# Optimization experiments

Hardware: AMD Instinct MI355X
Metric: run time of the kernel (lower is better)

Reference implementation:

```python
import jax, jax.numpy as jnp
import numpy as np

KSIZE = 5      # equivalent steerable kernel size
KMAX = 3       # max circular harmonic
STRIDE = 2
N_IN, N_OUT = 32, 16
B_TOTAL = 3 + 2 * KMAX  # 3 radial atoms at k=0, 2 per harmonic k>=1


def _make_basis():
    # Radial steerable base: Gaussian rings x circular harmonics cos(k*theta)/sin(k*theta)
    ys, xs = np.mgrid[:KSIZE, :KSIZE].astype(np.float64) - (KSIZE - 1) / 2
    r = np.sqrt(xs ** 2 + ys ** 2)
    th = np.arctan2(ys, xs)
    ring = lambda r0: np.exp(-(r - r0) ** 2 / (2 * 0.6 ** 2))
    b0 = np.stack([ring(r0) for r0 in (0.0, 1.0, 2.0)])          # (3, 5, 5)
    br, bi = [], []
    for k in range(1, KMAX + 1):
        br.append(np.stack([ring(r0) * np.cos(k * th) for r0 in (1.0, 2.0)]))  # (2,5,5)
        bi.append(np.stack([ring(r0) * np.sin(k * th) for r0 in (1.0, 2.0)]))
    return (b0.astype(np.float32),
            [b.astype(np.float32) for b in br],
            [b.astype(np.float32) for b in bi])


def _conv_transpose(x, w):
    # torch conv_transpose2d (stride=2, padding='same' -> pad=2, output_padding=1)
    # == dilated-input conv with spatially flipped kernel, explicit pad (2,3).
    rhs = jnp.flip(w, axis=(2, 3))  # (o, i, kh, kw)
    return jax.lax.conv_general_dilated(
        x, rhs, window_strides=(1, 1), padding=((2, 3), (2, 3)),
        lhs_dilation=(STRIDE, STRIDE),
        dimension_numbers=('NCHW', 'OIHW', 'NCHW'))


def setup_inputs() -> dict:
    key = jax.random.key(0)
    k1, k2, k3, k4 = jax.random.split(key, 4)
    x = jax.random.normal(k1, (8, N_IN, 192, 192), jnp.float32)
    # alpha[0]=cos-like, alpha[1]=sin-like field at output resolution; not unit-norm,
    # rho is derived from its norm (rho=None path of forward()).
    alpha = jax.random.normal(k2, (2, 8, 1, 384, 384), jnp.float32)
    weights = jax.random.normal(k3, (N_OUT, N_IN, B_TOTAL), jnp.float32) / np.sqrt(N_IN * B_TOTAL)
    bias = jax.random.normal(k4, (N_OUT,), jnp.float32) * 0.05
    return {"x": x, "alpha": alpha, "weights": weights, "bias": bias}


def reference(x, alpha, weights, bias):
    b0, br, bi = _make_basis()
    # normalize_vector: rho = |alpha|, alpha <- alpha / rho
    rho = jnp.sqrt(jnp.sum(alpha * alpha, axis=0))          # (b, 1, Ho, Wo)
    au = alpha / (rho[None] + 1e-8)
    c1, s1 = au[0], au[1]                                    # cos(a), sin(a)
    # k=0 term (rotation invariant)
    out = _conv_transpose(x, jnp.einsum('oib,bhw->oihw', weights[:, :, :3], jnp.asarray(b0)))
    ck, sk = c1, s1
    off = 3
    for k in range(KMAX):  # harmonics k=1..KMAX, steered by cos(k a), sin(k a)
        wk = weights[:, :, off:off + 2]
        off += 2
        Kr = jnp.einsum('oib,bhw->oihw', wk, jnp.asarray(br[k]))
        Ki = jnp.einsum('oib,bhw->oihw', wk, jnp.asarray(bi[k]))
        out = out + _conv_transpose(x, Kr) * ck + _conv_transpose(x, Ki) * sk
        ckn = ck * c1 - sk * s1  # Chebyshev-style recurrence for cos/sin of (k+1)a
        skn = sk * c1 + ck * s1
        ck, sk = ckn, skn
    return rho * out + bias[None, :, None, None]
```

## Files before the change

### kernel.cpp

```cpp
#include <hip/hip_runtime.h>

#define HIN 192
#define WOUT 384
#define NIN 32
#define NOUT 16
#define NSLOT 9
#define HP 194
#define HPLANE (HP * HP)
#define HQBATCH ((size_t)HPLANE * 18)

typedef float v2f __attribute__((ext_vector_type(2)));

__device__ __forceinline__ unsigned short f2bf(float f) {
    union { float f; unsigned int u; } v; v.f = f;
    unsigned int r = v.u + 0x7fffu + ((v.u >> 16) & 1u);
    return (unsigned short)(r >> 16);
}
__device__ __forceinline__ v2f up2(unsigned u) {
    v2f r;
    r.x = __uint_as_float(u << 16);
    r.y = __uint_as_float(u);
    return r;
}

__global__ __launch_bounds__(256) void kprep_w(const float* __restrict__ w, float* __restrict__ Wt) {
    int t = blockIdx.x * 256 + threadIdx.x;
    if (t >= NIN * NSLOT * NOUT) return;
    int c = t >> 8, r = t & 255;
    int i = r >> 3, j = r & 7;
    int m = c * 8 + j;
    int s = m >> 4, o = m & 15;
    Wt[t] = w[(o * NIN + i) * NSLOT + s];
}

__global__ __launch_bounds__(256) void kzero(uint4* __restrict__ hq, int nb) {
    int t = blockIdx.x * 256 + threadIdx.x;
    if (t >= nb * 772) return;
    int b = t / 772, r = t % 772;
    int iy, ix;
    if (r < 194)      { iy = 0;           ix = r; }
    else if (r < 388) { iy = 193;         ix = r - 194; }
    else if (r < 580) { iy = r - 388 + 1; ix = 0; }
    else              { iy = r - 580 + 1; ix = 193; }
    uint4* p = hq + (size_t)b * HQBATCH + iy * HP + ix;
    uint4 z; z.x = 0; z.y = 0; z.z = 0; z.w = 0;
    #pragma unroll
    for (int c = 0; c < 18; ++c) p[(size_t)c * HPLANE] = z;
}

__global__ __launch_bounds__(256) void kA(const float* __restrict__ x,
                                          const float* __restrict__ Wt,
                                          uint4* __restrict__ hq, int n0) {
    const int b = blockIdx.y;
    const int n = n0 + b;
    const int px = blockIdx.x * 256 + threadIdx.x;
    const int iy = px / HIN, ix = px % HIN;
    const float* xp = x + (size_t)n * NIN * HIN * HIN + px;
    float xv[NIN];
    #pragma unroll
    for (int i = 0; i < NIN; ++i) xv[i] = xp[(size_t)i * HIN * HIN];
    const int pos = (iy + 1) * HP + (ix + 1);
    uint4* hb = hq + (size_t)b * HQBATCH;
    #pragma unroll 1
    for (int c = 0; c < 18; ++c) {
        const float* wc = Wt + c * 256;
        float a[8];
        #pragma unroll
        for (int j = 0; j < 8; ++j) a[j] = 0.0f;
        #pragma unroll
        for (int i = 0; i < NIN; ++i) {
            const float xi = xv[i];
            #pragma unroll
            for (int j = 0; j < 8; ++j) a[j] = fmaf(wc[i * 8 + j], xi, a[j]);
        }
        uint4 v;
        v.x = (unsigned)f2bf(a[0]) | ((unsigned)f2bf(a[1]) << 16);
        v.y = (unsigned)f2bf(a[2]) | ((unsigned)f2bf(a[3]) << 16);
        v.z = (unsigned)f2bf(a[4]) | ((unsigned)f2bf(a[5]) << 16);
        v.w = (unsigned)f2bf(a[6]) | ((unsigned)f2bf(a[7]) << 16);
        hb[(size_t)c * HPLANE + pos] = v;
    }
}

template<int PY, int PX, int HF>
__device__ __forceinline__ void kb_body(const uint4* __restrict__ hb,
                                        const float* __restrict__ alpha,
                                        const float* __restrict__ bias_,
                                        float (&stage)[2][16][128],
                                        const float2 (&Cb)[NSLOT][25],
                                        int n, int Y, int X, int lane) {
    const int oy = 2 * Y + PY, ox = 2 * X + PX;
    const int aoff = (n * WOUT + oy) * WOUT + ox;
    const float a0 = alpha[aoff];
    const float a1 = alpha[(size_t)8 * WOUT * WOUT + aoff];
    const float rr = sqrtf(a0 * a0 + a1 * a1);
    const float inv = 1.0f / (rr + 1e-8f);
    float cc[3], ss[3];
    cc[0] = a0 * inv;                      ss[0] = a1 * inv;
    cc[1] = cc[0] * cc[0] - ss[0] * ss[0]; ss[1] = 2.0f * cc[0] * ss[0];
    cc[2] = cc[1] * cc[0] - ss[1] * ss[0]; ss[2] = ss[1] * cc[0] + cc[1] * ss[0];

    v2f acc2[4];
    #pragma unroll
    for (int j = 0; j < 4; ++j) { acc2[j].x = 0.0f; acc2[j].y = 0.0f; }

    #pragma unroll 1
    for (int ty = 0; ty < 3 - PY; ++ty) {
        const int piy = Y + 2 - ty;
        #pragma unroll 1
        for (int tx = 0; tx < 3 - PX; ++tx) {
            const int pix = X + 2 - tx;
            const int bi = (PY + 2 * ty) * 5 + (PX + 2 * tx);
            const unsigned pos = (unsigned)(piy * HP + pix);
            #pragma unroll
            for (int s = 0; s < NSLOT; ++s) {
                const float2 C = Cb[s][bi];
                float eb;
                if      (s < 3) eb = C.x;
                else if (s < 5) eb = C.x * cc[0] + C.y * ss[0];
                else if (s < 7) eb = C.x * cc[1] + C.y * ss[1];
                else            eb = C.x * cc[2] + C.y * ss[2];
                const uint4 v = hb[(size_t)(2 * s + HF) * HPLANE + pos];
                v2f e2; e2.x = eb; e2.y = eb;
                acc2[0] += e2 * up2(v.x);
                acc2[1] += e2 * up2(v.y);
                acc2[2] += e2 * up2(v.z);
                acc2[3] += e2 * up2(v.w);
            }
        }
    }

    #pragma unroll
    for (int j = 0; j < 4; ++j) {
        stage[PY][HF * 8 + 2 * j + 0][2 * lane + PX] = rr * acc2[j].x + bias_[HF * 8 + 2 * j + 0];
        stage[PY][HF * 8 + 2 * j + 1][2 * lane + PX] = rr * acc2[j].y + bias_[HF * 8 + 2 * j + 1];
    }
}

__global__ __launch_bounds__(512, 4) void kB(const uint4* __restrict__ hq,
                                             const float* __restrict__ alpha,
                                             const float* __restrict__ bias,
                                             float* __restrict__ out, int n0, int nb) {
    __shared__ float2 Cb[NSLOT][25];
    __shared__ float stage[2][16][128];
    {
        const int q = threadIdx.x;
        if (q < NSLOT * 25) {
            int s = q / 25, p = q % 25;
            int ky = p / 5, kx = p % 5;
            float ys = (float)(ky - 2), xs = (float)(kx - 2);
            float r = sqrtf(xs * xs + ys * ys);
            float th = atan2f(ys, xs);
            float cr, ci;
            if (s < 3) {
                float d = r - (float)s;
                cr = expf(-d * d * (1.0f / 0.72f));
                ci = 0.0f;
            } else {
                int k = (s - 3) / 2 + 1;
                float r0 = ((s - 3) & 1) ? 2.0f : 1.0f;
                float d = r - r0;
                float ring = expf(-d * d * (1.0f / 0.72f));
                float a = (float)k * th;
                cr = ring * cosf(a);
                ci = ring * sinf(a);
            }
            Cb[s][p] = make_float2(cr, ci);
        }
    }
    __syncthreads();

    const int tot = gridDim.x;
    const int cpx = tot >> 3;
    const int swz = ((int)blockIdx.x & 7) * cpx + ((int)blockIdx.x >> 3);
    const int Y = swz % 192;
    const int rest = swz / 192;
    const int b = rest % nb;
    const int bx = rest / nb;

    const int n = n0 + b;
    const int lane = threadIdx.x & 63;
    const int wv = threadIdx.x >> 6;
    const int X0 = bx * 64;
    const int X = X0 + lane;
    const uint4* hb = hq + (size_t)b * HQBATCH;

    switch (wv) {
        case 0: kb_body<0, 0, 0>(hb, alpha, bias, stage, Cb, n, Y, X, lane); break;
        case 1: kb_body<0, 1, 0>(hb, alpha, bias, stage, Cb, n, Y, X, lane); break;
        case 2: kb_body<1, 0, 0>(hb, alpha, bias, stage, Cb, n, Y, X, lane); break;
        case 3: kb_body<1, 1, 0>(hb, alpha, bias, stage, Cb, n, Y, X, lane); break;
        case 4: kb_body<0, 0, 1>(hb, alpha, bias, stage, Cb, n, Y, X, lane); break;
        case 5: kb_body<0, 1, 1>(hb, alpha, bias, stage, Cb, n, Y, X, lane); break;
        case 6: kb_body<1, 0, 1>(hb, alpha, bias, stage, Cb, n, Y, X, lane); break;
        default: kb_body<1, 1, 1>(hb, alpha, bias, stage, Cb, n, Y, X, lane); break;
    }

    __syncthreads();

    #pragma unroll
    for (int q = 0; q < 8; ++q) {
        const int f = q * 512 + threadIdx.x;
        const int row = f >> 7, col = f & 127;
        const int py = row >> 4, o = row & 15;
        out[(((size_t)n * NOUT + o) * WOUT + (2 * Y + py)) * WOUT + 2 * X0 + col]
            = stage[py][o][col];
    }
}

__global__ __launch_bounds__(256) void steered_convT(
    const float* __restrict__ x, const float* __restrict__ alpha,
    const float* __restrict__ weights, const float* __restrict__ bias,
    float* __restrict__ out) {
    __shared__ float sb[15 * 25];
    for (int q = threadIdx.x; q < 375; q += 256) {
        int s = q / 25, p = q % 25;
        int ky = p / 5, kx = p % 5;
        float ys = (float)(ky - 2), xs = (float)(kx - 2);
        float r = sqrtf(xs * xs + ys * ys);
        float th = atan2f(ys, xs);
        float val;
        if (s < 3) { float d = r - (float)s; val = expf(-d * d * (1.0f / 0.72f)); }
        else {
            int k = (s - 3) / 4 + 1; int rem = (s - 3) & 3;
            float r0 = (rem & 1) ? 2.0f : 1.0f; float d = r - r0;
            float ring = expf(-d * d * (1.0f / 0.72f));
            float ang = (float)k * th;
            val = ring * ((rem < 2) ? cosf(ang) : sinf(ang));
        }
        sb[q] = val;
    }
    __syncthreads();
    int idx = blockIdx.x * 256 + threadIdx.x;
    int ox = idx % WOUT; int tt = idx / WOUT; int oy = tt % WOUT; int n = tt / WOUT;
    const int plane = WOUT * WOUT;
    int aoff = (n * WOUT + oy) * WOUT + ox;
    float a0 = alpha[aoff], a1 = alpha[8 * plane + aoff];
    float rho = sqrtf(a0 * a0 + a1 * a1);
    float inv = 1.0f / (rho + 1e-8f);
    float c1 = a0 * inv, s1 = a1 * inv;
    float c2 = c1 * c1 - s1 * s1, s2 = 2.0f * s1 * c1;
    float c3 = c2 * c1 - s2 * s1, s3 = s2 * c1 + c2 * s1;
    int py = oy & 1, px = ox & 1;
    int iy0 = (oy >> 1) + 1, ix0 = (ox >> 1) + 1;
    float eb[9][9]; int off[9];
    #pragma unroll
    for (int t = 0; t < 9; ++t) {
        int ty = t / 3, tx = t % 3;
        int ky = py + 2 * ty, kx = px + 2 * tx;
        int iy = iy0 - ty, ix = ix0 - tx;
        bool v = (ky < 5) && (kx < 5) && (iy >= 0) && (iy < HIN) && (ix >= 0) && (ix < HIN);
        float m = v ? 1.0f : 0.0f;
        int ciy = min(max(iy, 0), HIN - 1), cix = min(max(ix, 0), HIN - 1);
        off[t] = ciy * HIN + cix;
        int bi_ = min(ky, 4) * 5 + min(kx, 4);
        eb[0][t] = sb[0 * 25 + bi_] * m;
        eb[1][t] = sb[1 * 25 + bi_] * m;
        eb[2][t] = sb[2 * 25 + bi_] * m;
        eb[3][t] = (sb[3 * 25 + bi_] * c1 + sb[5 * 25 + bi_] * s1) * m;
        eb[4][t] = (sb[4 * 25 + bi_] * c1 + sb[6 * 25 + bi_] * s1) * m;
        eb[5][t] = (sb[7 * 25 + bi_] * c2 + sb[9 * 25 + bi_] * s2) * m;
        eb[6][t] = (sb[8 * 25 + bi_] * c2 + sb[10 * 25 + bi_] * s2) * m;
        eb[7][t] = (sb[11 * 25 + bi_] * c3 + sb[13 * 25 + bi_] * s3) * m;
        eb[8][t] = (sb[12 * 25 + bi_] * c3 + sb[14 * 25 + bi_] * s3) * m;
    }
    float acc[NOUT];
    #pragma unroll
    for (int o = 0; o < NOUT; ++o) acc[o] = 0.0f;
    const float* xn = x + (size_t)n * NIN * HIN * HIN;
    for (int i = 0; i < NIN; ++i) {
        const float* xp = xn + (size_t)i * HIN * HIN;
        float tap[9];
        #pragma unroll
        for (int t = 0; t < 9; ++t) tap[t] = xp[off[t]];
        float G[9];
        #pragma unroll
        for (int b = 0; b < 9; ++b) {
            float s = 0.0f;
            #pragma unroll
            for (int t = 0; t < 9; ++t) s += eb[b][t] * tap[t];
            G[b] = s;
        }
        const float* wp = weights + i * 9;
        #pragma unroll
        for (int o = 0; o < NOUT; ++o) {
            float s = acc[o];
            #pragma unroll
            for (int b = 0; b < 9; ++b) s += wp[o * NIN * 9 + b] * G[b];
            acc[o] = s;
        }
    }
    #pragma unroll
    for (int o = 0; o < NOUT; ++o)
        out[((size_t)(n * NOUT + o) * WOUT + oy) * WOUT + ox] = rho * acc[o] + bias[o];
}

extern "C" void kernel_launch(void* const* d_in, const int* in_sizes, int n_in,
                              void* d_out, int out_size, void* d_ws, size_t ws_size,
                              hipStream_t stream) {
    const float* x       = (const float*)d_in[0];
    const float* alpha   = (const float*)d_in[1];
    const float* weights = (const float*)d_in[2];
    const float* bias    = (const float*)d_in[3];
    float* out = (float*)d_out;

    const size_t hoff = 32768;
    const size_t perb = HQBATCH * 16;
    int cb = 0;
    if (ws_size > hoff) cb = (int)((ws_size - hoff) / perb);
    if (cb > 8) cb = 8;

    if (cb < 1) {
        const int pixels = 8 * WOUT * WOUT;
        steered_convT<<<dim3(pixels / 256), 256, 0, stream>>>(x, alpha, weights, bias, out);
        return;
    }

    float* Wt = (float*)d_ws;
    uint4* hq = (uint4*)((char*)d_ws + hoff);

    kprep_w<<<dim3(18), 256, 0, stream>>>(weights, Wt);

    for (int n0 = 0; n0 < 8; n0 += cb) {
        int nb = 8 - n0; if (nb > cb) nb = cb;
        kzero<<<dim3((nb * 772 + 255) / 256), 256, 0, stream>>>(hq, nb);
        kA<<<dim3(144, nb), 256, 0, stream>>>(x, Wt, hq, n0);
        kB<<<dim3(576 * nb), 512, 0, stream>>>(hq, alpha, bias, out, n0, nb);
    }
}
```

Before: 150.1 us.

## Pair output parity classes per wave to share hq loads in kB

Each wave now computes two output parity phases, (0,AX) and (1,BX), that share the same input taps, so one uint4 load of the intermediate feeds both accumulators. Work per block falls from 8 waves to 4 and the block size drops from 512 to 256 threads. This is meant to cut redundant global/L2 loads of the bf16 intermediate. The cost is more registers and live accumulators per thread, plus branchy tap handling, which may lower occupancy.

Measured after the change: 139.0 us, median of 2. -7.4%, faster.

```diff
diff --git a/kernel.cpp b/kernel.cpp
--- a/kernel.cpp
+++ b/kernel.cpp
@@ -82,62 +82,100 @@
     }
 }
 
-template<int PY, int PX, int HF>
-__device__ __forceinline__ void kb_body(const uint4* __restrict__ hb,
+__device__ __forceinline__ void angles(const float* __restrict__ alpha, int n, int oy, int ox,
+                                       float (&cc)[3], float (&ss)[3], float& rr) {
+    const int aoff = (n * WOUT + oy) * WOUT + ox;
+    const float a0 = alpha[aoff];
+    const float a1 = alpha[(size_t)8 * WOUT * WOUT + aoff];
+    rr = sqrtf(a0 * a0 + a1 * a1);
+    const float inv = 1.0f / (rr + 1e-8f);
+    cc[0] = a0 * inv;                      ss[0] = a1 * inv;
+    cc[1] = cc[0] * cc[0] - ss[0] * ss[0]; ss[1] = 2.0f * cc[0] * ss[0];
+    cc[2] = cc[1] * cc[0] - ss[1] * ss[0]; ss[2] = ss[1] * cc[0] + cc[1] * ss[0];
+}
+
+__device__ __forceinline__ float ebv(const float2 C, int s,
+                                     const float (&cc)[3], const float (&ss)[3]) {
+    if (s < 3) return C.x;
+    if (s < 5) return C.x * cc[0] + C.y * ss[0];
+    if (s < 7) return C.x * cc[1] + C.y * ss[1];
+    return C.x * cc[2] + C.y * ss[2];
+}
+
+template<int PAIR, int HF>
+__device__ __forceinline__ void kb_pair(const uint4* __restrict__ hb,
                                         const float* __restrict__ alpha,
                                         const float* __restrict__ bias_,
                                         float (&stage)[2][16][128],
                                         const float2 (&Cb)[NSLOT][25],
                                         int n, int Y, int X, int lane) {
-    const int oy = 2 * Y + PY, ox = 2 * X + PX;
-    const int aoff = (n * WOUT + oy) * WOUT + ox;
-    const float a0 = alpha[aoff];
-    const float a1 = alpha[(size_t)8 * WOUT * WOUT + aoff];
-    const float rr = sqrtf(a0 * a0 + a1 * a1);
-    const float inv = 1.0f / (rr + 1e-8f);
-    float cc[3], ss[3];
-    cc[0] = a0 * inv;                      ss[0] = a1 * inv;
-    cc[1] = cc[0] * cc[0] - ss[0] * ss[0]; ss[1] = 2.0f * cc[0] * ss[0];
-    cc[2] = cc[1] * cc[0] - ss[1] * ss[0]; ss[2] = ss[1] * cc[0] + cc[1] * ss[0];
-
-    v2f acc2[4];
-    #pragma unroll
-    for (int j = 0; j < 4; ++j) { acc2[j].x = 0.0f; acc2[j].y = 0.0f; }
+    constexpr int AX = (PAIR == 0) ? 0 : 1;
+    constexpr int BX = (PAIR == 0) ? 1 : 0;
+
+    float ccA[3], ssA[3], ccB[3], ssB[3], rrA, rrB;
+    angles(alpha, n, 2 * Y + 0, 2 * X + AX, ccA, ssA, rrA);
+    angles(alpha, n, 2 * Y + 1, 2 * X + BX, ccB, ssB, rrB);
+
+    v2f aA[4], aB[4];
+    #pragma unroll
+    for (int j = 0; j < 4; ++j) { aA[j].x = 0.0f; aA[j].y = 0.0f; aB[j].x = 0.0f; aB[j].y = 0.0f; }
 
     #pragma unroll 1
-    for (int ty = 0; ty < 3 - PY; ++ty) {
+    for (int ty = 0; ty < 3; ++ty) {
         const int piy = Y + 2 - ty;
         #pragma unroll 1
-        for (int tx = 0; tx < 3 - PX; ++tx) {
+        for (int tx = 0; tx < 3; ++tx) {
+            const bool useA = (tx < 3 - AX);
+            const bool useB = (ty < 2) && (tx < 3 - BX);
+            if (!useA && !useB) continue;
             const int pix = X + 2 - tx;
-            const int bi = (PY + 2 * ty) * 5 + (PX + 2 * tx);
             const unsigned pos = (unsigned)(piy * HP + pix);
-            #pragma unroll
-            for (int s = 0; s < NSLOT; ++s) {
-                const float2 C = Cb[s][bi];
-                float eb;
-                if      (s < 3) eb = C.x;
-                else if (s < 5) eb = C.x * cc[0] + C.y * ss[0];
-                else if (s < 7) eb = C.x * cc[1] + C.y * ss[1];
-                else            eb = C.x * cc[2] + C.y * ss[2];
-                const uint4 v = hb[(size_t)(2 * s + HF) * HPLANE + pos];
-                v2f e2; e2.x = eb; e2.y = eb;
-                acc2[0] += e2 * up2(v.x);
-                acc2[1] += e2 * up2(v.y);
-                acc2[2] += e2 * up2(v.z);
-                acc2[3] += e2 * up2(v.w);
+            const int biA = (0 + 2 * ty) * 5 + (AX + 2 * tx);
+            const int biB = (1 + 2 * ty) * 5 + (BX + 2 * tx);
+            if (useA && useB) {
+                #pragma unroll
+                for (int s = 0; s < NSLOT; ++s) {
+                    const uint4 v = hb[(size_t)(2 * s + HF) * HPLANE + pos];
+                    const float eA = ebv(Cb[s][biA], s, ccA, ssA);
+                    const float eB = ebv(Cb[s][biB], s, ccB, ssB);
+                    v2f eA2; eA2.x = eA; eA2.y = eA;
+                    v2f eB2; eB2.x = eB; eB2.y = eB;
+                    v2f h0 = up2(v.x), h1 = up2(v.y), h2 = up2(v.z), h3 = up2(v.w);
+                    aA[0] += eA2 * h0; aA[1] += eA2 * h1; aA[2] += eA2 * h2; aA[3] += eA2 * h3;
+                    aB[0] += eB2 * h0; aB[1] += eB2 * h1; aB[2] += eB2 * h2; aB[3] += eB2 * h3;
+                }
+            } else if (useA) {
+                #pragma unroll
+                for (int s = 0; s < NSLOT; ++s) {
+                    const uint4 v = hb[(size_t)(2 * s + HF) * HPLANE + pos];
+                    const float eA = ebv(Cb[s][biA], s, ccA, ssA);
+                    v2f eA2; eA2.x = eA; eA2.y = eA;
+                    aA[0] += eA2 * up2(v.x); aA[1] += eA2 * up2(v.y);
+                    aA[2] += eA2 * up2(v.z); aA[3] += eA2 * up2(v.w);
+                }
+            } else {
+                #pragma unroll
+                for (int s = 0; s < NSLOT; ++s) {
+                    const uint4 v = hb[(size_t)(2 * s + HF) * HPLANE + pos];
+                    const float eB = ebv(Cb[s][biB], s, ccB, ssB);
+                    v2f eB2; eB2.x = eB; eB2.y = eB;
+                    aB[0] += eB2 * up2(v.x); aB[1] += eB2 * up2(v.y);
+                    aB[2] += eB2 * up2(v.z); aB[3] += eB2 * up2(v.w);
+                }
             }
         }
     }
 
     #pragma unroll
     for (int j = 0; j < 4; ++j) {
-        stage[PY][HF * 8 + 2 * j + 0][2 * lane + PX] = rr * acc2[j].x + bias_[HF * 8 + 2 * j + 0];
-        stage[PY][HF * 8 + 2 * j + 1][2 * lane + PX] = rr * acc2[j].y + bias_[HF * 8 + 2 * j + 1];
-    }
-}
-
-__global__ __launch_bounds__(512, 4) void kB(const uint4* __restrict__ hq,
+        stage[0][HF * 8 + 2 * j + 0][2 * lane + AX] = rrA * aA[j].x + bias_[HF * 8 + 2 * j + 0];
+        stage[0][HF * 8 + 2 * j + 1][2 * lane + AX] = rrA * aA[j].y + bias_[HF * 8 + 2 * j + 1];
+        stage[1][HF * 8 + 2 * j + 0][2 * lane + BX] = rrB * aB[j].x + bias_[HF * 8 + 2 * j + 0];
+        stage[1][HF * 8 + 2 * j + 1][2 * lane + BX] = rrB * aB[j].y + bias_[HF * 8 + 2 * j + 1];
+    }
+}
+
+__global__ __launch_bounds__(256, 4) void kB(const uint4* __restrict__ hq,
                                              const float* __restrict__ alpha,
                                              const float* __restrict__ bias,
                                              float* __restrict__ out, int n0, int nb) {
@@ -186,21 +224,17 @@
     const uint4* hb = hq + (size_t)b * HQBATCH;
 
     switch (wv) {
-        case 0: kb_body<0, 0, 0>(hb, alpha, bias, stage, Cb, n, Y, X, lane); break;
-        case 1: kb_body<0, 1, 0>(hb, alpha, bias, stage, Cb, n, Y, X, lane); break;
-        case 2: kb_body<1, 0, 0>(hb, alpha, bias, stage, Cb, n, Y, X, lane); break;
-        case 3: kb_body<1, 1, 0>(hb, alpha, bias, stage, Cb, n, Y, X, lane); break;
-        case 4: kb_body<0, 0, 1>(hb, alpha, bias, stage, Cb, n, Y, X, lane); break;
-        case 5: kb_body<0, 1, 1>(hb, alpha, bias, stage, Cb, n, Y, X, lane); break;
-        case 6: kb_body<1, 0, 1>(hb, alpha, bias, stage, Cb, n, Y, X, lane); break;
-        default: kb_body<1, 1, 1>(hb, alpha, bias, stage, Cb, n, Y, X, lane); break;
+        case 0: kb_pair<0, 0>(hb, alpha, bias, stage, Cb, n, Y, X, lane); break;
+        case 1: kb_pair<1, 0>(hb, alpha, bias, stage, Cb, n, Y, X, lane); break;
+        case 2: kb_pair<0, 1>(hb, alpha, bias, stage, Cb, n, Y, X, lane); break;
+        default: kb_pair<1, 1>(hb, alpha, bias, stage, Cb, n, Y, X, lane); break;
     }
 
     __syncthreads();
 
     #pragma unroll
-    for (int q = 0; q < 8; ++q) {
-        const int f = q * 512 + threadIdx.x;
+    for (int q = 0; q < 16; ++q) {
+        const int f = q * 256 + threadIdx.x;
         const int row = f >> 7, col = f & 127;
         const int py = row >> 4, o = row & 15;
         out[(((size_t)n * NOUT + o) * WOUT + (2 * Y + py)) * WOUT + 2 * X0 + col]
@@ -325,6 +359,6 @@
         int nb = 8 - n0; if (nb > cb) nb = cb;
         kzero<<<dim3((nb * 772 + 255) / 256), 256, 0, stream>>>(hq, nb);
         kA<<<dim3(144, nb), 256, 0, stream>>>(x, Wt, hq, n0);
-        kB<<<dim3(576 * nb), 512, 0, stream>>>(hq, alpha, bias, out, n0, nb);
-    }
-}
+        kB<<<dim3(576 * nb), 256, 0, stream>>>(hq, alpha, bias, out, n0, nb);
+    }
+}
```
